# Optimization experiments

Hardware: AMD Instinct MI355X
Metric: run time of the kernel (lower is better)

## Reference

```python
import jax, jax.numpy as jnp
import numpy as np

N = 30000
E = 480000
F_IN = 100
HID = 64
HEADS = 4
NCLS = 47
HC = HEADS * HID  # 256
NEG_SLOPE = 0.2
BN_EPS = 1e-5


def setup_inputs() -> dict:
    key = jax.random.key(0)
    ks = jax.random.split(key, 32)
    s = 0.1
    inp = {
        'x': jax.random.normal(ks[0], (N, F_IN), jnp.float32),
        'edge_index': jax.random.randint(ks[1], (2, E), 0, N, jnp.int32),
        # layer 0: GATConv(F_IN -> HID, heads, concat=True)
        'w0': jax.random.normal(ks[2], (F_IN, HC), jnp.float32) * s,
        'as0': jax.random.normal(ks[3], (HEADS, HID), jnp.float32) * s,
        'ad0': jax.random.normal(ks[4], (HEADS, HID), jnp.float32) * s,
        'b0': jnp.zeros((HC,), jnp.float32),
        'sw0': jax.random.normal(ks[5], (F_IN, HC), jnp.float32) * s,
        'sb0': jnp.zeros((HC,), jnp.float32),
        'g0': jnp.ones((HC,), jnp.float32),
        'be0': jnp.zeros((HC,), jnp.float32),
        # layer 1: GATConv(HC -> HID, heads, concat=True)
        'w1': jax.random.normal(ks[6], (HC, HC), jnp.float32) * s,
        'as1': jax.random.normal(ks[7], (HEADS, HID), jnp.float32) * s,
        'ad1': jax.random.normal(ks[8], (HEADS, HID), jnp.float32) * s,
        'b1': jnp.zeros((HC,), jnp.float32),
        'sw1': jax.random.normal(ks[9], (HC, HC), jnp.float32) * s,
        'sb1': jnp.zeros((HC,), jnp.float32),
        'g1': jnp.ones((HC,), jnp.float32),
        'be1': jnp.zeros((HC,), jnp.float32),
        # layer 2: GATConv(HC -> NCLS, heads, concat=False)
        'w2': jax.random.normal(ks[10], (HC, HEADS * NCLS), jnp.float32) * s,
        'as2': jax.random.normal(ks[11], (HEADS, NCLS), jnp.float32) * s,
        'ad2': jax.random.normal(ks[12], (HEADS, NCLS), jnp.float32) * s,
        'b2': jnp.zeros((NCLS,), jnp.float32),
        'sw2': jax.random.normal(ks[13], (HC, NCLS), jnp.float32) * s,
        'sb2': jnp.zeros((NCLS,), jnp.float32),
    }
    return inp


def gat_conv(x, src, dst, W, a_src, a_dst, bias, heads, out_ch, concat):
    # shared linear for src/dst (PyG GATConv with int in_channels)
    h = (x @ W).reshape(N, heads, out_ch)           # [N,H,C]
    al_s = jnp.sum(h * a_src, axis=-1)              # [N,H]
    al_d = jnp.sum(h * a_dst, axis=-1)              # [N,H]
    e = jax.nn.leaky_relu(al_s[src] + al_d[dst], NEG_SLOPE)  # [E,H]
    # segment (per-destination) softmax
    m = jax.ops.segment_max(e, dst, num_segments=N)
    e = jnp.exp(e - m[dst])
    den = jax.ops.segment_sum(e, dst, num_segments=N)
    alpha = e / (den[dst] + 1e-16)                  # [E,H]
    msg = h[src] * alpha[:, :, None]                # [E,H,C]
    out = jax.ops.segment_sum(msg, dst, num_segments=N)  # [N,H,C]
    out = out.reshape(N, heads * out_ch) if concat else out.mean(axis=1)
    return out + bias


def batch_norm(x, gamma, beta):
    mu = jnp.mean(x, axis=0)
    var = jnp.var(x, axis=0)
    return gamma * (x - mu) * jax.lax.rsqrt(var + BN_EPS) + beta


def reference(x, edge_index, w0, as0, ad0, b0, sw0, sb0, g0, be0,
              w1, as1, ad1, b1, sw1, sb1, g1, be1,
              w2, as2, ad2, b2, sw2, sb2):
    src, dst = edge_index[0], edge_index[1]
    # layer 0
    h = gat_conv(x, src, dst, w0, as0, ad0, b0, HEADS, HID, True)
    h = h + x @ sw0 + sb0
    h = jax.nn.elu(batch_norm(h, g0, be0))
    # layer 1
    h2 = gat_conv(h, src, dst, w1, as1, ad1, b1, HEADS, HID, True)
    h2 = h2 + h @ sw1 + sb1
    h2 = jax.nn.elu(batch_norm(h2, g1, be1))
    # layer 2 (concat=False -> mean over heads)
    out = gat_conv(h2, src, dst, w2, as2, ad2, b2, HEADS, NCLS, False)
    out = out + h2 @ sw2 + sb2
    return jax.nn.log_softmax(out, axis=-1)
```

## Files before the change

### kernel.cpp

```cpp
#include <hip/hip_runtime.h>
#include <math.h>

#define NN 30000
#define EE 480000
#define FIN 100
#define NCLS 47
#define NCOPY 16
#define SCAN_B 118

typedef unsigned short ushortt;
typedef __attribute__((ext_vector_type(8))) short bf16x8;
typedef __attribute__((ext_vector_type(8))) unsigned short us8;
typedef __attribute__((ext_vector_type(4))) float f32x4;
typedef __attribute__((ext_vector_type(2))) float f32x2;

__device__ unsigned char g_H8[(size_t)NN * 256];
__device__ ushortt g_Sb[(size_t)NN * 256];
__device__ float   g_S2[(size_t)NN * 48];
__device__ ushortt g_Fb[(size_t)NN * 256];
__device__ ushortt g_Xb[(size_t)NN * 128];
__device__ ushortt g_Wc0[512 * 128];
__device__ ushortt g_Wc1[512 * 256];
__device__ ushortt g_Wc2[235 * 256];
__device__ float g_als[NN * 4];
__device__ float g_ald[NN * 4];
__device__ int   g_rowptr[NN + 1];
__device__ int   g_counts[NN];
__device__ int   g_cur[NN];
__device__ int   g_bsum[128];
__device__ int   g_esrc[EE];
__device__ float g_stat[2 * NCOPY * 512];

__device__ __forceinline__ float wsum(float v) {
#pragma unroll
  for (int o = 32; o > 0; o >>= 1) v += __shfl_xor(v, o, 64);
  return v;
}
__device__ __forceinline__ float lrelu(float x) { return x > 0.f ? x : 0.2f * x; }
__device__ __forceinline__ ushortt f2bf(float f) {
  unsigned int u = __float_as_uint(f);
  unsigned int r = u + 0x7FFF + ((u >> 16) & 1);
  return (ushortt)(r >> 16);
}
__device__ __forceinline__ float bf2f(ushortt u) {
  return __uint_as_float(((unsigned int)u) << 16);
}
__device__ __forceinline__ unsigned int pk4_fp8(float f0, float f1, float f2, float f3) {
  unsigned int r = 0;
  r = __builtin_amdgcn_cvt_pk_fp8_f32(f0, f1, r, false);
  r = __builtin_amdgcn_cvt_pk_fp8_f32(f2, f3, r, true);
  return r;
}
__device__ __forceinline__ int swz(int row, int k) {
  return (k & ~63) | ((((k >> 3) & 7) ^ (row & 7)) << 3) | (k & 7);
}
__device__ __forceinline__ void glds16(const ushortt* gp, ushortt* lp) {
  __builtin_amdgcn_global_load_lds(
      (const __attribute__((address_space(1))) unsigned int*)gp,
      (__attribute__((address_space(3))) unsigned int*)lp, 16, 0, 0);
}

#define CW0 (512 * 128)
#define CW1 (512 * 256)
#define CW2 (235 * 256)
#define STATZ (2 * NCOPY * 512)
__global__ void conv_kernel(const float* __restrict__ w0, const float* __restrict__ sw0,
                            const float* __restrict__ w1, const float* __restrict__ sw1,
                            const float* __restrict__ w2, const float* __restrict__ sw2,
                            const float* __restrict__ x, const int* __restrict__ dst) {
  int i = blockIdx.x * blockDim.x + threadIdx.x;
  if (i < CW0) {
    int m = i >> 7, k = i & 127;
    float v = 0.f;
    if (k < FIN) v = (m < 256) ? w0[k * 256 + m] : sw0[k * 256 + (m - 256)];
    g_Wc0[(m << 7) | swz(m, k)] = f2bf(v);
    return;
  }
  i -= CW0;
  if (i < CW1) {
    int m = i >> 8, k = i & 255;
    float v = (m < 256) ? w1[k * 256 + m] : sw1[k * 256 + (m - 256)];
    g_Wc1[(m << 8) | swz(m, k)] = f2bf(v);
    return;
  }
  i -= CW1;
  if (i < CW2) {
    int m = i >> 8, k = i & 255;
    float v = (m < 188) ? w2[(size_t)k * 188 + m] : sw2[(size_t)k * 47 + (m - 188)];
    g_Wc2[(m << 8) | swz(m, k)] = f2bf(v);
    return;
  }
  i -= CW2;
  if (i < NN * 128) {
    int r = i >> 7, k = i & 127;
    g_Xb[(r << 7) | swz(r, k)] = (k < FIN) ? f2bf(x[r * FIN + k]) : 0;
    return;
  }
  i -= NN * 128;
  if (i < STATZ) {
    g_stat[i] = 0.f;
    return;
  }
  i -= STATZ;
  if (i < EE) atomicAdd(&g_counts[dst[i]], 1);
}

__global__ __launch_bounds__(256) void scan_a() {
  __shared__ int sh[256];
  int t = threadIdx.x;
  int i = blockIdx.x * 256 + t;
  int v = (i < NN) ? g_counts[i] : 0;
  sh[t] = v;
  __syncthreads();
  for (int off = 1; off < 256; off <<= 1) {
    int xv = (t >= off) ? sh[t - off] : 0;
    __syncthreads();
    sh[t] += xv;
    __syncthreads();
  }
  if (i < NN) {
    g_rowptr[i] = sh[t] - v;
    g_counts[i] = 0;
    g_cur[i] = 0;
  }
  if (t == 255) g_bsum[blockIdx.x] = sh[255];
}
__global__ __launch_bounds__(256) void scan_b() {
  __shared__ int sh[4];
  int t = threadIdx.x;
  int b = blockIdx.x;
  int v = (t < b) ? g_bsum[t] : 0;
  float fv = wsum((float)v);
  if ((t & 63) == 0) sh[t >> 6] = (int)fv;
  __syncthreads();
  int off = sh[0] + sh[1] + sh[2] + sh[3];
  int i = b * 256 + t;
  if (i < NN) g_rowptr[i] += off;
  if (i == NN - 1) g_rowptr[NN] = EE;
}
__global__ void scatter_kernel(const int* __restrict__ dst, const int* __restrict__ src) {
  int e = blockIdx.x * blockDim.x + threadIdx.x;
  if (e < EE) {
    int d = dst[e];
    int pos = g_rowptr[d] + atomicAdd(&g_cur[d], 1);
    g_esrc[pos] = src[e];
  }
}

__global__ __launch_bounds__(256) void mfma_gemm(
    const ushortt* __restrict__ A, const ushortt* __restrict__ Wt,
    unsigned char* __restrict__ out8, ushortt* __restrict__ out2b,
    float* __restrict__ out2f,
    int nrows, int Kp, int M, int S, int ld8, int ld2,
    const float* __restrict__ bias2, int pad47,
    const float* __restrict__ a_s, const float* __restrict__ a_d,
    float* __restrict__ alsp, float* __restrict__ aldp) {
  __shared__ __align__(16) ushortt smem[12288];
  ushortt* As = smem;
  ushortt* Ws = smem + 64 * 64;
  float* Ls = (float*)smem;
  int t = threadIdx.x;
  int wave = t >> 6, lane = t & 63;
  int row0 = blockIdx.y * 64, col0 = blockIdx.x * 128;
  int wr = wave >> 1, wc = wave & 1;
  int m16 = lane & 15, q = lane >> 4;
  int rin8 = lane >> 3;
  int koff = (lane & 7) * 8;

  f32x4 acc[2][4];
#pragma unroll
  for (int i = 0; i < 2; i++)
#pragma unroll
    for (int j = 0; j < 4; j++) acc[i][j] = (f32x4){0.f, 0.f, 0.f, 0.f};

  for (int k0 = 0; k0 < Kp; k0 += 64) {
#pragma unroll
    for (int r = 0; r < 2; r++) {
      int lrow = wave * 16 + r * 8;
      int ga = min(row0 + lrow + rin8, nrows - 1);
      glds16(A + (size_t)ga * Kp + k0 + koff, &As[lrow * 64]);
    }
#pragma unroll
    for (int r = 0; r < 4; r++) {
      int lrow = wave * 32 + r * 8;
      int gw = min(col0 + lrow + rin8, M - 1);
      glds16(Wt + (size_t)gw * Kp + k0 + koff, &Ws[lrow * 64]);
    }
    __syncthreads();
#pragma unroll
    for (int c = 0; c < 2; c++) {
      bf16x8 af[2], bf[4];
#pragma unroll
      for (int i = 0; i < 2; i++) {
        int row = wr * 32 + i * 16 + m16;
        int ch = (c * 4 + q) ^ (row & 7);
        af[i] = *(const bf16x8*)(&As[row * 64 + ch * 8]);
      }
#pragma unroll
      for (int i = 0; i < 4; i++) {
        int row = wc * 64 + i * 16 + m16;
        int ch = (c * 4 + q) ^ (row & 7);
        bf[i] = *(const bf16x8*)(&Ws[row * 64 + ch * 8]);
      }
#pragma unroll
      for (int rt = 0; rt < 2; rt++)
#pragma unroll
        for (int ct = 0; ct < 4; ct++)
          acc[rt][ct] = __builtin_amdgcn_mfma_f32_16x16x32_bf16(af[rt], bf[ct], acc[rt][ct], 0, 0, 0);
    }
    __syncthreads();
  }

  bool all1 = (!pad47) && (col0 + 128 <= S);
  bool all2 = (col0 >= S);
  int row8 = t >> 3, seg = t & 7;
#pragma unroll
  for (int p = 0; p < 2; p++) {
    __syncthreads();
    if (wr == p) {
#pragma unroll
      for (int rt = 0; rt < 2; rt++) {
#pragma unroll
        for (int ctt = 0; ctt < 4; ctt++) {
#pragma unroll
          for (int reg = 0; reg < 4; reg++) {
            int rloc = rt * 16 + q * 4 + reg;
            Ls[rloc * 132 + wc * 64 + ctt * 16 + m16] = acc[rt][ctt][reg];
          }
        }
      }
    }
    __syncthreads();
    int grow = row0 + p * 32 + row8;
    if (grow < nrows) {
      const float* lrow = Ls + row8 * 132 + seg * 16;
      int cbase = col0 + seg * 16;
      if (all1) {
        unsigned int q8[4];
#pragma unroll
        for (int kk = 0; kk < 4; kk++)
          q8[kk] = pk4_fp8(lrow[kk * 4], lrow[kk * 4 + 1], lrow[kk * 4 + 2], lrow[kk * 4 + 3]);
        uint4 v8 = {q8[0], q8[1], q8[2], q8[3]};
        *(uint4*)(out8 + (size_t)grow * ld8 + cbase) = v8;
        float s_p = 0.f, d_p = 0.f;
#pragma unroll
        for (int kk = 0; kk < 16; kk++) {
          s_p += lrow[kk] * a_s[cbase + kk];
          d_p += lrow[kk] * a_d[cbase + kk];
        }
        s_p += __shfl_xor(s_p, 1, 64); s_p += __shfl_xor(s_p, 2, 64);
        d_p += __shfl_xor(d_p, 1, 64); d_p += __shfl_xor(d_p, 2, 64);
        if ((seg & 3) == 0) {
          int head = cbase >> 6;
          alsp[grow * 4 + head] = s_p;
          aldp[grow * 4 + head] = d_p;
        }
      } else if (all2) {
        const float* brow = bias2 + (cbase - S);
        ushortt* orow = out2b + (size_t)grow * ld2 + (cbase - S);
        unsigned int pk[8];
#pragma unroll
        for (int kk = 0; kk < 8; kk++) {
          unsigned int lo = f2bf(lrow[kk * 2] + brow[kk * 2]);
          unsigned int hi = f2bf(lrow[kk * 2 + 1] + brow[kk * 2 + 1]);
          pk[kk] = lo | (hi << 16);
        }
        uint4 v0 = {pk[0], pk[1], pk[2], pk[3]};
        uint4 v1 = {pk[4], pk[5], pk[6], pk[7]};
        *(uint4*)(orow) = v0;
        *(uint4*)(orow + 8) = v1;
      } else {
        float pa0 = 0.f, pa1 = 0.f, pd0 = 0.f, pd1 = 0.f;
        int h0 = cbase / 47;
        for (int kk = 0; kk < 16; kk++) {
          int c = cbase + kk;
          if (c >= M) break;
          float v = lrow[kk];
          if (c < S) {
            int hd = c / 47, ch = c - hd * 47;
            int c1 = hd * 48 + ch;
            out8[(size_t)grow * ld8 + c1] =
                (unsigned char)(pk4_fp8(v, 0.f, 0.f, 0.f) & 0xFF);
            if (ch == 46) out8[(size_t)grow * ld8 + c1 + 1] = 0;
            float sw = a_s[hd * 47 + ch], dw = a_d[hd * 47 + ch];
            if (hd == h0) { pa0 += v * sw; pd0 += v * dw; }
            else { pa1 += v * sw; pd1 += v * dw; }
          } else {
            out2f[(size_t)grow * ld2 + (c - S)] = v + bias2[c - S];
          }
        }
        if (pad47 && cbase < S) {
          if (pa0 != 0.f || pd0 != 0.f) {
            atomicAdd(&alsp[grow * 4 + h0], pa0);
            atomicAdd(&aldp[grow * 4 + h0], pd0);
          }
          if ((pa1 != 0.f || pd1 != 0.f) && h0 + 1 < 4) {
            atomicAdd(&alsp[grow * 4 + h0 + 1], pa1);
            atomicAdd(&aldp[grow * 4 + h0 + 1], pd1);
          }
        }
      }
    }
  }
}

__global__ __launch_bounds__(256) void attn_kernel(const unsigned char* __restrict__ H8,
                                                   const float* __restrict__ bias,
                                                   ushortt* __restrict__ Sb,
                                                   float* __restrict__ statp) {
  __shared__ __align__(16) float p_sh[4 * 256];
  __shared__ int s_sh[4 * 64];
  __shared__ float rs_[4 * 256];
  __shared__ float rq_[4 * 256];
  int w = threadIdx.x >> 6, lane = threadIdx.x & 63;
  int n = blockIdx.x * 4 + w;
  float* pw = p_sh + w * 256;
  int* sw_ = s_sh + w * 64;
  int rs = g_rowptr[n], deg = g_rowptr[n + 1] - rs;
  float4 ald = *(const float4*)(g_ald + n * 4);
  int q = lane >> 4;
  float den0 = 0, den1 = 0, den2 = 0, den3 = 0;
  float a0 = 0, a1 = 0, a2 = 0, a3 = 0;
  for (int base = 0; base < deg; base += 64) {
    int j = base + lane;
    float p0 = 0, p1 = 0, p2 = 0, p3 = 0;
    int s = 0;
    if (j < deg) {
      s = g_esrc[rs + j];
      float4 av = *(const float4*)(g_als + s * 4);
      p0 = __expf(lrelu(av.x + ald.x)); den0 += p0;
      p1 = __expf(lrelu(av.y + ald.y)); den1 += p1;
      p2 = __expf(lrelu(av.z + ald.z)); den2 += p2;
      p3 = __expf(lrelu(av.w + ald.w)); den3 += p3;
    }
    pw[lane * 4 + 0] = p0; pw[lane * 4 + 1] = p1;
    pw[lane * 4 + 2] = p2; pw[lane * 4 + 3] = p3;
    sw_[lane] = s;
    int cnt = min(64, deg - base);
    for (int jj = 0; jj < cnt; jj++) {
      int ss = sw_[jj];
      float p = pw[jj * 4 + q];
      unsigned int hv = *(const unsigned int*)(H8 + (size_t)ss * 256 + 4 * lane);
      f32x2 lo = __builtin_amdgcn_cvt_pk_f32_fp8(hv, false);
      f32x2 hi = __builtin_amdgcn_cvt_pk_f32_fp8(hv, true);
      a0 += p * lo.x;
      a1 += p * lo.y;
      a2 += p * hi.x;
      a3 += p * hi.y;
    }
  }
  den0 = wsum(den0); den1 = wsum(den1); den2 = wsum(den2); den3 = wsum(den3);
  float denq = (q == 0) ? den0 : (q == 1) ? den1 : (q == 2) ? den2 : den3;
  float inv = 1.f / (denq + 1e-16f);
  size_t o = (size_t)n * 256 + 4 * lane;
  ushort4 sv = *(const ushort4*)(Sb + o);
  float4 bv = *(const float4*)(bias + 4 * lane);
  ushort4 ov;
  ov.x = f2bf(a0 * inv + bv.x + bf2f(sv.x));
  ov.y = f2bf(a1 * inv + bv.y + bf2f(sv.y));
  ov.z = f2bf(a2 * inv + bv.z + bf2f(sv.z));
  ov.w = f2bf(a3 * inv + bv.w + bf2f(sv.w));
  *(ushort4*)(Sb + o) = ov;
  float v0 = bf2f(ov.x), v1 = bf2f(ov.y), v2 = bf2f(ov.z), v3 = bf2f(ov.w);
  int cb = w * 256 + 4 * lane;
  rs_[cb + 0] = v0; rs_[cb + 1] = v1; rs_[cb + 2] = v2; rs_[cb + 3] = v3;
  rq_[cb + 0] = v0 * v0; rq_[cb + 1] = v1 * v1; rq_[cb + 2] = v2 * v2; rq_[cb + 3] = v3 * v3;
  __syncthreads();
  int c = threadIdx.x;
  float s = rs_[c] + rs_[256 + c] + rs_[512 + c] + rs_[768 + c];
  float qq = rq_[c] + rq_[256 + c] + rq_[512 + c] + rq_[768 + c];
  int copy = blockIdx.x & (NCOPY - 1);
  atomicAdd(&statp[copy * 512 + c], s);
  atomicAdd(&statp[copy * 512 + 256 + c], qq);
}

__global__ __launch_bounds__(256) void attn2_kernel(const unsigned char* __restrict__ H8,
                                                    const float* __restrict__ bias,
                                                    const float* __restrict__ S2,
                                                    float* __restrict__ out) {
  __shared__ __align__(16) float p_sh[4 * 256];
  __shared__ int s_sh[4 * 64];
  __shared__ float xh[4][4][48];
  int w = threadIdx.x >> 6, lane = threadIdx.x & 63;
  int n = blockIdx.x * 4 + w;
  float* pw = p_sh + w * 256;
  int* sw_ = s_sh + w * 64;
  int rs = g_rowptr[n], deg = g_rowptr[n + 1] - rs;
  float4 ald = *(const float4*)(g_ald + n * 4);
  int head = lane / 12;
  float den0 = 0, den1 = 0, den2 = 0, den3 = 0;
  float a0 = 0, a1 = 0, a2 = 0, a3 = 0;
  for (int base = 0; base < deg; base += 64) {
    int j = base + lane;
    float p0 = 0, p1 = 0, p2 = 0, p3 = 0;
    int s = 0;
    if (j < deg) {
      s = g_esrc[rs + j];
      float4 av = *(const float4*)(g_als + s * 4);
      p0 = __expf(lrelu(av.x + ald.x)); den0 += p0;
      p1 = __expf(lrelu(av.y + ald.y)); den1 += p1;
      p2 = __expf(lrelu(av.z + ald.z)); den2 += p2;
      p3 = __expf(lrelu(av.w + ald.w)); den3 += p3;
    }
    pw[lane * 4 + 0] = p0; pw[lane * 4 + 1] = p1;
    pw[lane * 4 + 2] = p2; pw[lane * 4 + 3] = p3;
    sw_[lane] = s;
    int cnt = min(64, deg - base);
    if (lane < 48) {
      for (int jj = 0; jj < cnt; jj++) {
        int ss = sw_[jj];
        float p = pw[jj * 4 + head];
        unsigned int hv = *(const unsigned int*)(H8 + (size_t)ss * 192 + lane * 4);
        f32x2 lo = __builtin_amdgcn_cvt_pk_f32_fp8(hv, false);
        f32x2 hi = __builtin_amdgcn_cvt_pk_f32_fp8(hv, true);
        a0 += p * lo.x;
        a1 += p * lo.y;
        a2 += p * hi.x;
        a3 += p * hi.y;
      }
    }
  }
  den0 = wsum(den0); den1 = wsum(den1); den2 = wsum(den2); den3 = wsum(den3);
  if (lane < 48) {
    float dh = (head == 0) ? den0 : (head == 1) ? den1 : (head == 2) ? den2 : den3;
    float inv = 1.f / (dh + 1e-16f);
    int chin = (lane % 12) * 4;
    xh[w][head][chin + 0] = a0 * inv;
    xh[w][head][chin + 1] = a1 * inv;
    xh[w][head][chin + 2] = a2 * inv;
    xh[w][head][chin + 3] = a3 * inv;
  }
  float v = 0.f;
  if (lane < NCLS)
    v = 0.25f * (xh[w][0][lane] + xh[w][1][lane] + xh[w][2][lane] + xh[w][3][lane]) +
        bias[lane] + S2[(size_t)n * NCLS + lane];
  float mv = (lane < NCLS) ? v : -INFINITY;
#pragma unroll
  for (int o = 32; o > 0; o >>= 1) mv = fmaxf(mv, __shfl_xor(mv, o, 64));
  float ex = (lane < NCLS) ? __expf(v - mv) : 0.f;
  float s = wsum(ex);
  if (lane < NCLS) out[(size_t)n * NCLS + lane] = v - mv - logf(s);
}

__global__ __launch_bounds__(256) void bn_norm_kernel(const ushortt* __restrict__ Sb,
                                                      const float* __restrict__ gamma,
                                                      const float* __restrict__ beta,
                                                      const float* __restrict__ statp,
                                                      float* __restrict__ zs,
                                                      float* __restrict__ zd) {
  __shared__ float sc_sh[256], off_sh[256];
  int t = threadIdx.x;
  float s = 0.f, qq = 0.f;
#pragma unroll
  for (int k = 0; k < NCOPY; k++) {
    s += statp[k * 512 + t];
    qq += statp[k * 512 + 256 + t];
  }
  float mu = s * (1.f / NN);
  float var = qq * (1.f / NN) - mu * mu;
  float rg = rsqrtf(var + 1e-5f) * gamma[t];
  sc_sh[t] = rg;
  off_sh[t] = beta[t] - mu * rg;
  __syncthreads();
  if (zs) {
    for (int i = blockIdx.x * 256 + t; i < NN * 4; i += gridDim.x * 256) {
      zs[i] = 0.f;
      zd[i] = 0.f;
    }
  }
  int rows = (NN + gridDim.x - 1) / gridDim.x;
  int r0 = blockIdx.x * rows, r1 = min(r0 + rows, NN);
  int chunk = t & 31;
  int ro = t >> 5;
  float scv[8], ofv[8];
#pragma unroll
  for (int k = 0; k < 8; k++) {
    scv[k] = sc_sh[chunk * 8 + k];
    ofv[k] = off_sh[chunk * 8 + k];
  }
  for (int r = r0 + ro; r < r1; r += 8) {
    us8 xv = *(const us8*)(Sb + (size_t)r * 256 + chunk * 8);
    us8 yv;
#pragma unroll
    for (int k = 0; k < 8; k++) {
      float v = bf2f((ushortt)xv[k]) * scv[k] + ofv[k];
      v = v > 0.f ? v : (__expf(v) - 1.f);
      yv[k] = f2bf(v);
    }
    int c8 = (chunk & 24) | ((chunk & 7) ^ (r & 7));
    *(us8*)(g_Fb + ((size_t)r << 8) + c8 * 8) = yv;
  }
}

extern "C" void kernel_launch(void* const* d_in, const int* in_sizes, int n_in,
                              void* d_out, int out_size, void* d_ws, size_t ws_size,
                              hipStream_t stream) {
  const float* x = (const float*)d_in[0];
  const int* ei = (const int*)d_in[1];
  const int* src = ei;
  const int* dst = ei + EE;
  const float* w0 = (const float*)d_in[2];
  const float* as0 = (const float*)d_in[3];
  const float* ad0 = (const float*)d_in[4];
  const float* b0 = (const float*)d_in[5];
  const float* sw0 = (const float*)d_in[6];
  const float* sb0 = (const float*)d_in[7];
  const float* gm0 = (const float*)d_in[8];
  const float* be0 = (const float*)d_in[9];
  const float* w1 = (const float*)d_in[10];
  const float* as1 = (const float*)d_in[11];
  const float* ad1 = (const float*)d_in[12];
  const float* b1 = (const float*)d_in[13];
  const float* sw1 = (const float*)d_in[14];
  const float* sb1 = (const float*)d_in[15];
  const float* gm1 = (const float*)d_in[16];
  const float* be1 = (const float*)d_in[17];
  const float* w2 = (const float*)d_in[18];
  const float* as2 = (const float*)d_in[19];
  const float* ad2 = (const float*)d_in[20];
  const float* b2 = (const float*)d_in[21];
  const float* sw2 = (const float*)d_in[22];
  const float* sb2 = (const float*)d_in[23];
  float* out = (float*)d_out;

  ushortt *Sb, *Fb, *Xb, *Wc0, *Wc1, *Wc2;
  unsigned char* H8;
  float *S2, *als, *ald, *stat;
  hipGetSymbolAddress((void**)&H8, HIP_SYMBOL(g_H8));
  hipGetSymbolAddress((void**)&Sb, HIP_SYMBOL(g_Sb));
  hipGetSymbolAddress((void**)&S2, HIP_SYMBOL(g_S2));
  hipGetSymbolAddress((void**)&Fb, HIP_SYMBOL(g_Fb));
  hipGetSymbolAddress((void**)&Xb, HIP_SYMBOL(g_Xb));
  hipGetSymbolAddress((void**)&Wc0, HIP_SYMBOL(g_Wc0));
  hipGetSymbolAddress((void**)&Wc1, HIP_SYMBOL(g_Wc1));
  hipGetSymbolAddress((void**)&Wc2, HIP_SYMBOL(g_Wc2));
  hipGetSymbolAddress((void**)&als, HIP_SYMBOL(g_als));
  hipGetSymbolAddress((void**)&ald, HIP_SYMBOL(g_ald));
  hipGetSymbolAddress((void**)&stat, HIP_SYMBOL(g_stat));

  const int convN = CW0 + CW1 + CW2 + NN * 128 + STATZ + EE;
  conv_kernel<<<(convN + 255) / 256, 256, 0, stream>>>(w0, sw0, w1, sw1, w2, sw2, x, dst);

  scan_a<<<SCAN_B, 256, 0, stream>>>();
  scan_b<<<SCAN_B, 256, 0, stream>>>();
  scatter_kernel<<<(EE + 255) / 256, 256, 0, stream>>>(dst, src);

  const int gy = (NN + 63) / 64;
  const int ga = NN / 4;

  mfma_gemm<<<dim3(4, gy), 256, 0, stream>>>(Xb, Wc0, H8, Sb, nullptr, NN, 128, 512, 256,
                                             256, 256, sb0, 0, as0, ad0, als, ald);
  attn_kernel<<<ga, 256, 0, stream>>>(H8, b0, Sb, stat);
  bn_norm_kernel<<<480, 256, 0, stream>>>(Sb, gm0, be0, stat, nullptr, nullptr);

  mfma_gemm<<<dim3(4, gy), 256, 0, stream>>>(Fb, Wc1, H8, Sb, nullptr, NN, 256, 512, 256,
                                             256, 256, sb1, 0, as1, ad1, als, ald);
  attn_kernel<<<ga, 256, 0, stream>>>(H8, b1, Sb, stat + NCOPY * 512);
  bn_norm_kernel<<<480, 256, 0, stream>>>(Sb, gm1, be1, stat + NCOPY * 512, als, ald);

  mfma_gemm<<<dim3(2, gy), 256, 0, stream>>>(Fb, Wc2, H8, nullptr, S2, NN, 256, 235, 188,
                                             192, 47, sb2, 1, as2, ad2, als, ald);
  attn2_kernel<<<ga, 256, 0, stream>>>(H8, b2, S2, out);
}
```

Before: 385.3 us.

## Gather four edges per wavefront with 16-byte FP8 loads and shuffle reduction

In both attention aggregation kernels, the wavefront is split into four 16-lane groups. Each group handles a different neighbour edge, and each lane loads 16 FP8 bytes instead of 4. Partial sums for 16 channels per lane are then combined across groups with cross-lane shuffles before normalisation. The goal is fewer, wider gather loads and more independent memory requests in flight per loop step. The cost is 16 accumulators per lane, extra shuffle work, and runtime-indexed register arrays that could spill to scratch.

```diff
diff --git a/kernel.cpp b/kernel.cpp
--- a/kernel.cpp
+++ b/kernel.cpp
@@ -318,9 +318,12 @@
   int* sw_ = s_sh + w * 64;
   int rs = g_rowptr[n], deg = g_rowptr[n + 1] - rs;
   float4 ald = *(const float4*)(g_ald + n * 4);
-  int q = lane >> 4;
+  int g = lane >> 4;
+  int m = lane & 15;
   float den0 = 0, den1 = 0, den2 = 0, den3 = 0;
-  float a0 = 0, a1 = 0, a2 = 0, a3 = 0;
+  float a[16];
+#pragma unroll
+  for (int k = 0; k < 16; k++) a[k] = 0.f;
   for (int base = 0; base < deg; base += 64) {
     int j = base + lane;
     float p0 = 0, p1 = 0, p2 = 0, p3 = 0;
@@ -337,32 +340,45 @@
     pw[lane * 4 + 2] = p2; pw[lane * 4 + 3] = p3;
     sw_[lane] = s;
     int cnt = min(64, deg - base);
-    for (int jj = 0; jj < cnt; jj++) {
-      int ss = sw_[jj];
-      float p = pw[jj * 4 + q];
-      unsigned int hv = *(const unsigned int*)(H8 + (size_t)ss * 256 + 4 * lane);
-      f32x2 lo = __builtin_amdgcn_cvt_pk_f32_fp8(hv, false);
-      f32x2 hi = __builtin_amdgcn_cvt_pk_f32_fp8(hv, true);
-      a0 += p * lo.x;
-      a1 += p * lo.y;
-      a2 += p * hi.x;
-      a3 += p * hi.y;
+    for (int jj = 0; jj < cnt; jj += 4) {
+      int j4 = jj + g;
+      int ss = sw_[j4];
+      float p = pw[j4 * 4 + (m >> 2)];
+      uint4 hv = *(const uint4*)(H8 + (size_t)ss * 256 + m * 16);
+      unsigned int hw[4] = {hv.x, hv.y, hv.z, hv.w};
+#pragma unroll
+      for (int u = 0; u < 4; u++) {
+        f32x2 lo = __builtin_amdgcn_cvt_pk_f32_fp8(hw[u], false);
+        f32x2 hi = __builtin_amdgcn_cvt_pk_f32_fp8(hw[u], true);
+        a[u * 4 + 0] += p * lo.x;
+        a[u * 4 + 1] += p * lo.y;
+        a[u * 4 + 2] += p * hi.x;
+        a[u * 4 + 3] += p * hi.y;
+      }
     }
   }
   den0 = wsum(den0); den1 = wsum(den1); den2 = wsum(den2); den3 = wsum(den3);
-  float denq = (q == 0) ? den0 : (q == 1) ? den1 : (q == 2) ? den2 : den3;
+#pragma unroll
+  for (int k = 0; k < 16; k++) {
+    a[k] += __shfl_xor(a[k], 16, 64);
+    a[k] += __shfl_xor(a[k], 32, 64);
+  }
+  int off = g * 4;
+  int cb2 = m * 16 + off;
+  int head = m >> 2;
+  float denq = (head == 0) ? den0 : (head == 1) ? den1 : (head == 2) ? den2 : den3;
   float inv = 1.f / (denq + 1e-16f);
-  size_t o = (size_t)n * 256 + 4 * lane;
+  size_t o = (size_t)n * 256 + cb2;
   ushort4 sv = *(const ushort4*)(Sb + o);
-  float4 bv = *(const float4*)(bias + 4 * lane);
+  float4 bv = *(const float4*)(bias + cb2);
   ushort4 ov;
-  ov.x = f2bf(a0 * inv + bv.x + bf2f(sv.x));
-  ov.y = f2bf(a1 * inv + bv.y + bf2f(sv.y));
-  ov.z = f2bf(a2 * inv + bv.z + bf2f(sv.z));
-  ov.w = f2bf(a3 * inv + bv.w + bf2f(sv.w));
+  ov.x = f2bf(a[off + 0] * inv + bv.x + bf2f(sv.x));
+  ov.y = f2bf(a[off + 1] * inv + bv.y + bf2f(sv.y));
+  ov.z = f2bf(a[off + 2] * inv + bv.z + bf2f(sv.z));
+  ov.w = f2bf(a[off + 3] * inv + bv.w + bf2f(sv.w));
   *(ushort4*)(Sb + o) = ov;
   float v0 = bf2f(ov.x), v1 = bf2f(ov.y), v2 = bf2f(ov.z), v3 = bf2f(ov.w);
-  int cb = w * 256 + 4 * lane;
+  int cb = w * 256 + cb2;
   rs_[cb + 0] = v0; rs_[cb + 1] = v1; rs_[cb + 2] = v2; rs_[cb + 3] = v3;
   rq_[cb + 0] = v0 * v0; rq_[cb + 1] = v1 * v1; rq_[cb + 2] = v2 * v2; rq_[cb + 3] = v3 * v3;
   __syncthreads();
@@ -387,9 +403,14 @@
   int* sw_ = s_sh + w * 64;
   int rs = g_rowptr[n], deg = g_rowptr[n + 1] - rs;
   float4 ald = *(const float4*)(g_ald + n * 4);
-  int head = lane / 12;
+  int g = lane >> 4;
+  int m = lane & 15;
+  int mc = min(m, 11);
+  int headm = mc / 3;
   float den0 = 0, den1 = 0, den2 = 0, den3 = 0;
-  float a0 = 0, a1 = 0, a2 = 0, a3 = 0;
+  float a[16];
+#pragma unroll
+  for (int k = 0; k < 16; k++) a[k] = 0.f;
   for (int base = 0; base < deg; base += 64) {
     int j = base + lane;
     float p0 = 0, p1 = 0, p2 = 0, p3 = 0;
@@ -406,29 +427,40 @@
     pw[lane * 4 + 2] = p2; pw[lane * 4 + 3] = p3;
     sw_[lane] = s;
     int cnt = min(64, deg - base);
-    if (lane < 48) {
-      for (int jj = 0; jj < cnt; jj++) {
-        int ss = sw_[jj];
-        float p = pw[jj * 4 + head];
-        unsigned int hv = *(const unsigned int*)(H8 + (size_t)ss * 192 + lane * 4);
-        f32x2 lo = __builtin_amdgcn_cvt_pk_f32_fp8(hv, false);
-        f32x2 hi = __builtin_amdgcn_cvt_pk_f32_fp8(hv, true);
-        a0 += p * lo.x;
-        a1 += p * lo.y;
-        a2 += p * hi.x;
-        a3 += p * hi.y;
+    for (int jj = 0; jj < cnt; jj += 4) {
+      int j4 = jj + g;
+      int ss = sw_[j4];
+      float p = (m < 12) ? pw[j4 * 4 + headm] : 0.f;
+      uint4 hv = *(const uint4*)(H8 + (size_t)ss * 192 + mc * 16);
+      unsigned int hw[4] = {hv.x, hv.y, hv.z, hv.w};
+#pragma unroll
+      for (int u = 0; u < 4; u++) {
+        f32x2 lo = __builtin_amdgcn_cvt_pk_f32_fp8(hw[u], false);
+        f32x2 hi = __builtin_amdgcn_cvt_pk_f32_fp8(hw[u], true);
+        a[u * 4 + 0] += p * lo.x;
+        a[u * 4 + 1] += p * lo.y;
+        a[u * 4 + 2] += p * hi.x;
+        a[u * 4 + 3] += p * hi.y;
       }
     }
   }
   den0 = wsum(den0); den1 = wsum(den1); den2 = wsum(den2); den3 = wsum(den3);
-  if (lane < 48) {
-    float dh = (head == 0) ? den0 : (head == 1) ? den1 : (head == 2) ? den2 : den3;
+#pragma unroll
+  for (int k = 0; k < 16; k++) {
+    a[k] += __shfl_xor(a[k], 16, 64);
+    a[k] += __shfl_xor(a[k], 32, 64);
+  }
+  if (m < 12) {
+    int off = g * 4;
+    int c192 = m * 16 + off;
+    int hd = c192 / 48;
+    int chin = c192 - hd * 48;
+    float dh = (hd == 0) ? den0 : (hd == 1) ? den1 : (hd == 2) ? den2 : den3;
     float inv = 1.f / (dh + 1e-16f);
-    int chin = (lane % 12) * 4;
-    xh[w][head][chin + 0] = a0 * inv;
-    xh[w][head][chin + 1] = a1 * inv;
-    xh[w][head][chin + 2] = a2 * inv;
-    xh[w][head][chin + 3] = a3 * inv;
+    xh[w][hd][chin + 0] = a[off + 0] * inv;
+    xh[w][hd][chin + 1] = a[off + 1] * inv;
+    xh[w][hd][chin + 2] = a[off + 2] * inv;
+    xh[w][hd][chin + 3] = a[off + 3] * inv;
   }
   float v = 0.f;
   if (lane < NCLS)
```

Result: no change. 379.1 us, median of 2 (-1.6%).
